# Performance work log

Measured on AMD Instinct MI355X. Metric: run time of the kernel, lower is better.

## Reference

```python
import jax, jax.numpy as jnp
import numpy as np

MARGIN = 0.3
NUM_CLASSES = 1000


def setup_inputs() -> dict:
    key = jax.random.key(0)
    k1, k2 = jax.random.split(key)
    B, D = 8192, 256
    inputs = jax.random.normal(k1, (B, D), dtype=jnp.float32)
    targets = jax.random.randint(k2, (B,), 0, NUM_CLASSES, dtype=jnp.int64)
    return {"inputs": inputs, "targets": targets}


def reference(inputs, targets):
    # Squared Euclidean pairwise distances: ||x_i||^2 + ||x_j||^2 - 2 x_i.x_j
    sq = jnp.sum(inputs * inputs, axis=1)                      # [B]
    dist = sq[:, None] + sq[None, :] - 2.0 * (inputs @ inputs.T)  # [B, B]

    # Hard mining: per-row max over positives (same label, incl. self),
    # min over negatives, exactly as the torch per-row masked max/min loop.
    pos_mask = targets[:, None] == targets[None, :]            # [B, B] bool
    neg_inf = jnp.float32(-jnp.inf)
    pos_inf = jnp.float32(jnp.inf)
    dist_ap = jnp.max(jnp.where(pos_mask, dist, neg_inf), axis=1)  # [B]
    dist_an = jnp.min(jnp.where(pos_mask, pos_inf, dist), axis=1)  # [B]

    # MarginRankingLoss(margin)(dist_an, dist_ap, y=1) = mean relu(ap - an + m)
    loss = jnp.mean(jax.nn.relu(dist_ap - dist_an + MARGIN))
    prec = jnp.mean((dist_an > dist_ap).astype(jnp.float32))
    return (loss, prec)
```

## Files before the change

kernel.cpp:

```cpp
#include <hip/hip_runtime.h>
#include <hip/hip_bf16.h>

#define B_N 8192
#define D_K 256
#define MARGIN 0.3f
#define NBLK 2080

typedef float f32x4 __attribute__((ext_vector_type(4)));
typedef short s16x8 __attribute__((ext_vector_type(8)));

__device__ __forceinline__ unsigned fkey(float f) {
    unsigned u = __float_as_uint(f);
    return (u & 0x80000000u) ? ~u : (u | 0x80000000u);
}
__device__ __forceinline__ float kval(unsigned k) {
    return (k & 0x80000000u) ? __uint_as_float(k ^ 0x80000000u)
                             : __uint_as_float(~k);
}

__device__ __forceinline__ void load_lds16(const unsigned short* g,
                                           unsigned short* l) {
    __builtin_amdgcn_global_load_lds(
        (const __attribute__((address_space(1))) unsigned int*)g,
        (__attribute__((address_space(3))) unsigned int*)l, 16, 0, 0);
}

__device__ __forceinline__ float rowred_max(float v) {
    v = fmaxf(v, __int_as_float(__builtin_amdgcn_update_dpp(
            __float_as_int(v), __float_as_int(v), 0x118, 0xF, 0xF, false)));
    v = fmaxf(v, __int_as_float(__builtin_amdgcn_update_dpp(
            __float_as_int(v), __float_as_int(v), 0x114, 0xF, 0xF, false)));
    v = fmaxf(v, __int_as_float(__builtin_amdgcn_update_dpp(
            __float_as_int(v), __float_as_int(v), 0x112, 0xF, 0xF, false)));
    v = fmaxf(v, __int_as_float(__builtin_amdgcn_update_dpp(
            __float_as_int(v), __float_as_int(v), 0x111, 0xF, 0xF, false)));
    return v;
}
__device__ __forceinline__ float rowred_min(float v) {
    v = fminf(v, __int_as_float(__builtin_amdgcn_update_dpp(
            __float_as_int(v), __float_as_int(v), 0x118, 0xF, 0xF, false)));
    v = fminf(v, __int_as_float(__builtin_amdgcn_update_dpp(
            __float_as_int(v), __float_as_int(v), 0x114, 0xF, 0xF, false)));
    v = fminf(v, __int_as_float(__builtin_amdgcn_update_dpp(
            __float_as_int(v), __float_as_int(v), 0x112, 0xF, 0xF, false)));
    v = fminf(v, __int_as_float(__builtin_amdgcn_update_dpp(
            __float_as_int(v), __float_as_int(v), 0x111, 0xF, 0xF, false)));
    return v;
}

__global__ __launch_bounds__(256) void prep_kernel(const float* __restrict__ X,
        float* __restrict__ sq, unsigned* __restrict__ apk,
        unsigned* __restrict__ ank, unsigned short* __restrict__ Xp,
        float* __restrict__ acc2) {
    int row  = (blockIdx.x << 2) + (threadIdx.x >> 6);
    int lane = threadIdx.x & 63;
    const float4 v = reinterpret_cast<const float4*>(X + (size_t)row * D_K)[lane];

    float xs[4] = {v.x, v.y, v.z, v.w};
    ushort4 hv;
    unsigned short* hp = &hv.x;
    float s = 0.f;
    #pragma unroll
    for (int i = 0; i < 4; ++i) {
        __hip_bfloat16 h = __float2bfloat16(xs[i]);
        hp[i] = *reinterpret_cast<unsigned short*>(&h);
        float hf = __bfloat162float(h);
        s = fmaf(hf, hf, s);
    }
    *reinterpret_cast<ushort4*>(Xp + (size_t)row * D_K + lane * 4) = hv;

    #pragma unroll
    for (int o = 32; o > 0; o >>= 1) s += __shfl_down(s, o, 64);
    if (lane == 0) {
        sq[row]  = s;
        apk[row] = 0u;
        ank[row] = 0xFFFFFFFFu;
    }
    if (blockIdx.x == 0 && threadIdx.x == 0) {
        acc2[0] = 0.f; acc2[1] = 0.f;
        reinterpret_cast<unsigned*>(acc2)[2] = 0u;
    }
}

#define BM 128
#define BN 128

__global__ __launch_bounds__(256, 4) void dist_kernel(
        const unsigned short* __restrict__ Xp,
        const int* __restrict__ tgt, const float* __restrict__ sq,
        unsigned* __restrict__ apk, unsigned* __restrict__ ank) {
    __shared__ unsigned short Ab[2][128 * 32];
    __shared__ unsigned short Bb[2][128 * 32];

    const int t    = threadIdx.x;
    const int lane = t & 63;
    const int wave = t >> 6;
    const int wrow = (wave >> 1) * 64;
    const int wcol = (wave & 1) * 64;
    const int fr   = lane & 15;
    const int quad = lane >> 4;
    const float INF = __int_as_float(0x7f800000);

    int tt = blockIdx.x;
    int bx = (int)((sqrtf(8.f * (float)tt + 1.f) - 1.f) * 0.5f);
    while ((bx + 1) * (bx + 2) / 2 <= tt) ++bx;
    while (bx * (bx + 1) / 2 > tt) --bx;
    int by = tt - bx * (bx + 1) / 2;
    const int bm = by * BM;
    const int bn = bx * BN;

    const unsigned short* ag[2];
    const unsigned short* bg[2];
    int ldso[2];
    #pragma unroll
    for (int j = 0; j < 2; ++j) {
        int S   = wave * 64 + j * 256 + lane;
        int l   = S >> 3, idx = S & 7;
        int u   = idx >> 1, r = l * 2 + (idx & 1);
        ag[j]   = Xp + (size_t)(bm + r) * D_K + u * 8;
        bg[j]   = Xp + (size_t)(bn + r) * D_K + u * 8;
        ldso[j] = S * 8;
    }

    f32x4 acc[4][4];
    #pragma unroll
    for (int i = 0; i < 4; ++i)
        #pragma unroll
        for (int j = 0; j < 4; ++j) acc[i][j] = (f32x4){0.f, 0.f, 0.f, 0.f};

    #pragma unroll
    for (int j = 0; j < 2; ++j) {
        load_lds16(ag[j], &Ab[0][ldso[j]]);
        load_lds16(bg[j], &Bb[0][ldso[j]]);
    }

    #pragma unroll 1
    for (int w = 0; w < 8; ++w) {
        __syncthreads();
        if (w < 7) {
            const int ko = (w + 1) * 32;
            #pragma unroll
            for (int j = 0; j < 2; ++j) {
                load_lds16(ag[j] + ko, &Ab[(w + 1) & 1][ldso[j]]);
                load_lds16(bg[j] + ko, &Bb[(w + 1) & 1][ldso[j]]);
            }
        }
        const unsigned short* At = Ab[w & 1];
        const unsigned short* Bt = Bb[w & 1];

        s16x8 a[4], b[4];
        #pragma unroll
        for (int mi = 0; mi < 4; ++mi) {
            int R = wrow + mi * 16 + fr;
            int S = (R >> 1) * 8 + quad * 2 + (R & 1);
            a[mi] = *reinterpret_cast<const s16x8*>(&At[S * 8]);
        }
        #pragma unroll
        for (int ni = 0; ni < 4; ++ni) {
            int R = wcol + ni * 16 + fr;
            int S = (R >> 1) * 8 + quad * 2 + (R & 1);
            b[ni] = *reinterpret_cast<const s16x8*>(&Bt[S * 8]);
        }
        #pragma unroll
        for (int mi = 0; mi < 4; ++mi)
            #pragma unroll
            for (int ni = 0; ni < 4; ++ni)
                acc[mi][ni] = __builtin_amdgcn_mfma_f32_16x16x32_bf16(
                    a[mi], b[ni], acc[mi][ni], 0, 0, 0);
    }

    int   ct[4]; float csq[4];
    #pragma unroll
    for (int ni = 0; ni < 4; ++ni) {
        int c = bn + wcol + ni * 16 + fr;
        ct[ni] = tgt[c]; csq[ni] = sq[c];
    }
    float cap[4], can[4];
    #pragma unroll
    for (int ni = 0; ni < 4; ++ni) { cap[ni] = -INF; can[ni] = INF; }

    #pragma unroll
    for (int mi = 0; mi < 4; ++mi) {
        #pragma unroll
        for (int reg = 0; reg < 4; ++reg) {
            int rl = wrow + mi * 16 + quad * 4 + reg;
            int rt = tgt[bm + rl]; float rsq = sq[bm + rl];
            float rap = -INF, ran = INF;
            #pragma unroll
            for (int ni = 0; ni < 4; ++ni) {
                float d = rsq + csq[ni] - 2.f * acc[mi][ni][reg];
                bool pos = (rt == ct[ni]);
                if (pos) { rap = fmaxf(rap, d); cap[ni] = fmaxf(cap[ni], d); }
                else     { ran = fminf(ran, d); can[ni] = fminf(can[ni], d); }
            }
            rap = rowred_max(rap);
            ran = rowred_min(ran);
            if (fr == 15) {
                atomicMax(&apk[bm + rl], fkey(rap));
                atomicMin(&ank[bm + rl], fkey(ran));
            }
        }
    }
    #pragma unroll
    for (int ni = 0; ni < 4; ++ni) {
        #pragma unroll
        for (int o = 16; o < 64; o <<= 1) {
            cap[ni] = fmaxf(cap[ni], __shfl_xor(cap[ni], o, 64));
            can[ni] = fminf(can[ni], __shfl_xor(can[ni], o, 64));
        }
    }
    if (lane < 16) {
        #pragma unroll
        for (int ni = 0; ni < 4; ++ni) {
            int c = bn + wcol + ni * 16 + lane;
            atomicMax(&apk[c], fkey(cap[ni]));
            atomicMin(&ank[c], fkey(can[ni]));
        }
    }
}

__global__ __launch_bounds__(256) void final_kernel(const unsigned* __restrict__ apk,
        const unsigned* __restrict__ ank, float* __restrict__ acc2,
        float* __restrict__ out) {
    __shared__ float s_sum[4], s_cnt[4];
    int i = blockIdx.x * 256 + threadIdx.x;
    float ap = kval(apk[i]);
    float an = kval(ank[i]);
    float v  = ap - an + MARGIN;
    float sum = v > 0.f ? v : 0.f;
    float cnt = an > ap ? 1.f : 0.f;
    #pragma unroll
    for (int o = 32; o > 0; o >>= 1) {
        sum += __shfl_down(sum, o, 64);
        cnt += __shfl_down(cnt, o, 64);
    }
    int wave = threadIdx.x >> 6, lane = threadIdx.x & 63;
    if (lane == 0) { s_sum[wave] = sum; s_cnt[wave] = cnt; }
    __syncthreads();
    if (threadIdx.x == 0) {
        float ts = 0.f, tc = 0.f;
        #pragma unroll
        for (int w = 0; w < 4; ++w) { ts += s_sum[w]; tc += s_cnt[w]; }
        atomicAdd(&acc2[0], ts);
        atomicAdd(&acc2[1], tc);
        __threadfence();
        unsigned ticket = atomicAdd(reinterpret_cast<unsigned*>(acc2) + 2, 1u);
        if (ticket == gridDim.x - 1) {
            float fs = atomicAdd(&acc2[0], 0.f);
            float fc = atomicAdd(&acc2[1], 0.f);
            out[0] = fs / (float)B_N;
            out[1] = fc / (float)B_N;
        }
    }
}

extern "C" void kernel_launch(void* const* d_in, const int* in_sizes, int n_in,
                              void* d_out, int out_size, void* d_ws, size_t ws_size,
                              hipStream_t stream) {
    const float* X   = (const float*)d_in[0];
    const int*   tgt = (const int*)d_in[1];

    char* ws = (char*)d_ws;
    float*          sq   = (float*)ws;
    unsigned*       apk  = (unsigned*)(ws + 32768);
    unsigned*       ank  = (unsigned*)(ws + 65536);
    float*          acc2 = (float*)(ws + 98304);
    unsigned short* Xp   = (unsigned short*)(ws + 131072);

    float* out = (float*)d_out;

    prep_kernel<<<B_N / 4, 256, 0, stream>>>(X, sq, apk, ank, Xp, acc2);
    dist_kernel<<<NBLK, 256, 0, stream>>>(Xp, tgt, sq, apk, ank);
    final_kernel<<<B_N / 256, 256, 0, stream>>>(apk, ank, acc2, out);
}
```

Before: 120.2 us.

## Process two triangular tiles per block with continuous prefetch across tiles

Each dist_kernel block now handles two consecutive upper-triangular 128x128 tiles instead of one, halving the grid to 1040 blocks. The k-loop runs 16 steps, so the first K-chunk of the second tile is prefetched into LDS during the last step of the first tile, and the epilogue for the first tile runs while that load is in flight. This is meant to amortize block launch and prologue cost and hide load latency at tile boundaries. In exchange there are fewer blocks to spread over the CUs, which may hurt load balance, and the epilogue inside the loop may raise register pressure.

```diff
diff --git a/kernel.cpp b/kernel.cpp
--- a/kernel.cpp
+++ b/kernel.cpp
@@ -4,7 +4,7 @@
 #define B_N 8192
 #define D_K 256
 #define MARGIN 0.3f
-#define NBLK 2080
+#define NBLK2 1040
 
 typedef float f32x4 __attribute__((ext_vector_type(4)));
 typedef short s16x8 __attribute__((ext_vector_type(8)));
@@ -101,53 +101,64 @@
     const int quad = lane >> 4;
     const float INF = __int_as_float(0x7f800000);
 
-    int tt = blockIdx.x;
+    int tt = blockIdx.x * 2;
     int bx = (int)((sqrtf(8.f * (float)tt + 1.f) - 1.f) * 0.5f);
     while ((bx + 1) * (bx + 2) / 2 <= tt) ++bx;
     while (bx * (bx + 1) / 2 > tt) --bx;
     int by = tt - bx * (bx + 1) / 2;
-    const int bm = by * BM;
-    const int bn = bx * BN;
-
-    const unsigned short* ag[2];
-    const unsigned short* bg[2];
+    int bmA[2], bnA[2];
+    bmA[0] = by * BM; bnA[0] = bx * BN;
+    if (by < bx) { bmA[1] = (by + 1) * BM; bnA[1] = bx * BN; }
+    else         { bmA[1] = 0;             bnA[1] = (bx + 1) * BN; }
+
+    int rgo[2];
+    int ugo[2];
     int ldso[2];
     #pragma unroll
     for (int j = 0; j < 2; ++j) {
         int S   = wave * 64 + j * 256 + lane;
         int l   = S >> 3, idx = S & 7;
-        int u   = idx >> 1, r = l * 2 + (idx & 1);
-        ag[j]   = Xp + (size_t)(bm + r) * D_K + u * 8;
-        bg[j]   = Xp + (size_t)(bn + r) * D_K + u * 8;
+        rgo[j]  = l * 2 + (idx & 1);
+        ugo[j]  = (idx >> 1) * 8;
         ldso[j] = S * 8;
     }
 
     f32x4 acc[4][4];
-    #pragma unroll
-    for (int i = 0; i < 4; ++i)
-        #pragma unroll
-        for (int j = 0; j < 4; ++j) acc[i][j] = (f32x4){0.f, 0.f, 0.f, 0.f};
 
     #pragma unroll
     for (int j = 0; j < 2; ++j) {
-        load_lds16(ag[j], &Ab[0][ldso[j]]);
-        load_lds16(bg[j], &Bb[0][ldso[j]]);
+        load_lds16(Xp + (size_t)(bmA[0] + rgo[j]) * D_K + ugo[j],
+                   &Ab[0][ldso[j]]);
+        load_lds16(Xp + (size_t)(bnA[0] + rgo[j]) * D_K + ugo[j],
+                   &Bb[0][ldso[j]]);
     }
 
     #pragma unroll 1
-    for (int w = 0; w < 8; ++w) {
+    for (int widx = 0; widx < 16; ++widx) {
+        const int w = widx & 7;
         __syncthreads();
-        if (w < 7) {
-            const int ko = (w + 1) * 32;
+        if (widx < 15) {
+            const int nx = widx + 1;
+            const int nt = nx >> 3;
+            const int ko = (nx & 7) * 32;
             #pragma unroll
             for (int j = 0; j < 2; ++j) {
-                load_lds16(ag[j] + ko, &Ab[(w + 1) & 1][ldso[j]]);
-                load_lds16(bg[j] + ko, &Bb[(w + 1) & 1][ldso[j]]);
-            }
-        }
-        const unsigned short* At = Ab[w & 1];
-        const unsigned short* Bt = Bb[w & 1];
-
+                load_lds16(Xp + (size_t)(bmA[nt] + rgo[j]) * D_K + ko + ugo[j],
+                           &Ab[nx & 1][ldso[j]]);
+                load_lds16(Xp + (size_t)(bnA[nt] + rgo[j]) * D_K + ko + ugo[j],
+                           &Bb[nx & 1][ldso[j]]);
+            }
+        }
+        if (w == 0) {
+            #pragma unroll
+            for (int i = 0; i < 4; ++i)
+                #pragma unroll
+                for (int j = 0; j < 4; ++j)
+                    acc[i][j] = (f32x4){0.f, 0.f, 0.f, 0.f};
+        }
+
+        const unsigned short* At = Ab[widx & 1];
+        const unsigned short* Bt = Bb[widx & 1];
         s16x8 a[4], b[4];
         #pragma unroll
         for (int mi = 0; mi < 4; ++mi) {
@@ -167,54 +178,58 @@
             for (int ni = 0; ni < 4; ++ni)
                 acc[mi][ni] = __builtin_amdgcn_mfma_f32_16x16x32_bf16(
                     a[mi], b[ni], acc[mi][ni], 0, 0, 0);
-    }
-
-    int   ct[4]; float csq[4];
-    #pragma unroll
-    for (int ni = 0; ni < 4; ++ni) {
-        int c = bn + wcol + ni * 16 + fr;
-        ct[ni] = tgt[c]; csq[ni] = sq[c];
-    }
-    float cap[4], can[4];
-    #pragma unroll
-    for (int ni = 0; ni < 4; ++ni) { cap[ni] = -INF; can[ni] = INF; }
-
-    #pragma unroll
-    for (int mi = 0; mi < 4; ++mi) {
-        #pragma unroll
-        for (int reg = 0; reg < 4; ++reg) {
-            int rl = wrow + mi * 16 + quad * 4 + reg;
-            int rt = tgt[bm + rl]; float rsq = sq[bm + rl];
-            float rap = -INF, ran = INF;
+
+        if (w == 7) {
+            const int bm = bmA[widx >> 3];
+            const int bn = bnA[widx >> 3];
+            int   ct[4]; float csq[4];
             #pragma unroll
             for (int ni = 0; ni < 4; ++ni) {
-                float d = rsq + csq[ni] - 2.f * acc[mi][ni][reg];
-                bool pos = (rt == ct[ni]);
-                if (pos) { rap = fmaxf(rap, d); cap[ni] = fmaxf(cap[ni], d); }
-                else     { ran = fminf(ran, d); can[ni] = fminf(can[ni], d); }
-            }
-            rap = rowred_max(rap);
-            ran = rowred_min(ran);
-            if (fr == 15) {
-                atomicMax(&apk[bm + rl], fkey(rap));
-                atomicMin(&ank[bm + rl], fkey(ran));
-            }
-        }
-    }
-    #pragma unroll
-    for (int ni = 0; ni < 4; ++ni) {
-        #pragma unroll
-        for (int o = 16; o < 64; o <<= 1) {
-            cap[ni] = fmaxf(cap[ni], __shfl_xor(cap[ni], o, 64));
-            can[ni] = fminf(can[ni], __shfl_xor(can[ni], o, 64));
-        }
-    }
-    if (lane < 16) {
-        #pragma unroll
-        for (int ni = 0; ni < 4; ++ni) {
-            int c = bn + wcol + ni * 16 + lane;
-            atomicMax(&apk[c], fkey(cap[ni]));
-            atomicMin(&ank[c], fkey(can[ni]));
+                int c = bn + wcol + ni * 16 + fr;
+                ct[ni] = tgt[c]; csq[ni] = sq[c];
+            }
+            float cap[4], can[4];
+            #pragma unroll
+            for (int ni = 0; ni < 4; ++ni) { cap[ni] = -INF; can[ni] = INF; }
+
+            #pragma unroll
+            for (int mi = 0; mi < 4; ++mi) {
+                #pragma unroll
+                for (int reg = 0; reg < 4; ++reg) {
+                    int rl = wrow + mi * 16 + quad * 4 + reg;
+                    int rt = tgt[bm + rl]; float rsq = sq[bm + rl];
+                    float rap = -INF, ran = INF;
+                    #pragma unroll
+                    for (int ni = 0; ni < 4; ++ni) {
+                        float d = rsq + csq[ni] - 2.f * acc[mi][ni][reg];
+                        bool pos = (rt == ct[ni]);
+                        if (pos) { rap = fmaxf(rap, d); cap[ni] = fmaxf(cap[ni], d); }
+                        else     { ran = fminf(ran, d); can[ni] = fminf(can[ni], d); }
+                    }
+                    rap = rowred_max(rap);
+                    ran = rowred_min(ran);
+                    if (fr == 15) {
+                        atomicMax(&apk[bm + rl], fkey(rap));
+                        atomicMin(&ank[bm + rl], fkey(ran));
+                    }
+                }
+            }
+            #pragma unroll
+            for (int ni = 0; ni < 4; ++ni) {
+                #pragma unroll
+                for (int o = 16; o < 64; o <<= 1) {
+                    cap[ni] = fmaxf(cap[ni], __shfl_xor(cap[ni], o, 64));
+                    can[ni] = fminf(can[ni], __shfl_xor(can[ni], o, 64));
+                }
+            }
+            if (lane < 16) {
+                #pragma unroll
+                for (int ni = 0; ni < 4; ++ni) {
+                    int c = bn + wcol + ni * 16 + lane;
+                    atomicMax(&apk[c], fkey(cap[ni]));
+                    atomicMin(&ank[c], fkey(can[ni]));
+                }
+            }
         }
     }
 }
@@ -270,6 +285,6 @@
     float* out = (float*)d_out;
 
     prep_kernel<<<B_N / 4, 256, 0, stream>>>(X, sq, apk, ank, Xp, acc2);
-    dist_kernel<<<NBLK, 256, 0, stream>>>(Xp, tgt, sq, apk, ank);
+    dist_kernel<<<NBLK2, 256, 0, stream>>>(Xp, tgt, sq, apk, ank);
     final_kernel<<<B_N / 256, 256, 0, stream>>>(apk, ank, acc2, out);
 }
```

After: 131.4 us. 9.3% more time.

## Use single-wave 64x64 triangular tiles with XOR-swizzled LDS and no block barriers

Applied to the files above, without the earlier changes.

The distance kernel moves from 256-thread blocks on 128x128 tiles to 64-thread single-wave blocks on 64x64 tiles, so the triangular grid grows from 2080 to 8256 tiles. Because each block is one wave, __syncthreads is replaced by explicit s_waitcnt on vmcnt/lgkmcnt, and the last K-step is peeled out of the loop. LDS gets an XOR swizzle to cut bank conflicts. Smaller tiles mean less operand reuse per tile, more global/L2 traffic and roughly twice as many epilogue atomics, traded for finer-grained parallelism and no barrier cost.

```diff
diff --git a/kernel.cpp b/kernel.cpp
--- a/kernel.cpp
+++ b/kernel.cpp
@@ -4,7 +4,7 @@
 #define B_N 8192
 #define D_K 256
 #define MARGIN 0.3f
-#define NBLK 2080
+#define NT 8256
 
 typedef float f32x4 __attribute__((ext_vector_type(4)));
 typedef short s16x8 __attribute__((ext_vector_type(8)));
@@ -82,21 +82,14 @@
     }
 }
 
-#define BM 128
-#define BN 128
-
-__global__ __launch_bounds__(256, 4) void dist_kernel(
+__global__ __launch_bounds__(64, 2) void dist_kernel(
         const unsigned short* __restrict__ Xp,
         const int* __restrict__ tgt, const float* __restrict__ sq,
         unsigned* __restrict__ apk, unsigned* __restrict__ ank) {
-    __shared__ unsigned short Ab[2][128 * 32];
-    __shared__ unsigned short Bb[2][128 * 32];
-
-    const int t    = threadIdx.x;
-    const int lane = t & 63;
-    const int wave = t >> 6;
-    const int wrow = (wave >> 1) * 64;
-    const int wcol = (wave & 1) * 64;
+    __shared__ __attribute__((aligned(16))) unsigned short Ab[2][64 * 32];
+    __shared__ __attribute__((aligned(16))) unsigned short Bb[2][64 * 32];
+
+    const int lane = threadIdx.x;
     const int fr   = lane & 15;
     const int quad = lane >> 4;
     const float INF = __int_as_float(0x7f800000);
@@ -106,22 +99,34 @@
     while ((bx + 1) * (bx + 2) / 2 <= tt) ++bx;
     while (bx * (bx + 1) / 2 > tt) --bx;
     int by = tt - bx * (bx + 1) / 2;
-    const int bm = by * BM;
-    const int bn = bx * BN;
-
-    const unsigned short* ag[2];
-    const unsigned short* bg[2];
-    int ldso[2];
-    #pragma unroll
-    for (int j = 0; j < 2; ++j) {
-        int S   = wave * 64 + j * 256 + lane;
-        int l   = S >> 3, idx = S & 7;
-        int u   = idx >> 1, r = l * 2 + (idx & 1);
-        ag[j]   = Xp + (size_t)(bm + r) * D_K + u * 8;
-        bg[j]   = Xp + (size_t)(bn + r) * D_K + u * 8;
+    const int bm = by * 64;
+    const int bn = bx * 64;
+
+    const unsigned short* ag[4];
+    const unsigned short* bg[4];
+    int ldso[4];
+    #pragma unroll
+    for (int j = 0; j < 4; ++j) {
+        int S = j * 64 + lane;
+        int r = S >> 2;
+        int q = (S & 3) ^ ((r >> 2) & 3);
+        ag[j]   = Xp + (size_t)(bm + r) * D_K + q * 8;
+        bg[j]   = Xp + (size_t)(bn + r) * D_K + q * 8;
         ldso[j] = S * 8;
     }
 
+    int afo[4], bfo[4];
+    #pragma unroll
+    for (int mi = 0; mi < 4; ++mi) {
+        int R = mi * 16 + fr;
+        afo[mi] = (R * 4 + (quad ^ ((R >> 2) & 3))) * 8;
+    }
+    #pragma unroll
+    for (int ni = 0; ni < 4; ++ni) {
+        int R = ni * 16 + fr;
+        bfo[ni] = (R * 4 + (quad ^ ((R >> 2) & 3))) * 8;
+    }
+
     f32x4 acc[4][4];
     #pragma unroll
     for (int i = 0; i < 4; ++i)
@@ -129,38 +134,31 @@
         for (int j = 0; j < 4; ++j) acc[i][j] = (f32x4){0.f, 0.f, 0.f, 0.f};
 
     #pragma unroll
-    for (int j = 0; j < 2; ++j) {
+    for (int j = 0; j < 4; ++j) {
         load_lds16(ag[j], &Ab[0][ldso[j]]);
         load_lds16(bg[j], &Bb[0][ldso[j]]);
     }
 
     #pragma unroll 1
-    for (int w = 0; w < 8; ++w) {
-        __syncthreads();
-        if (w < 7) {
-            const int ko = (w + 1) * 32;
-            #pragma unroll
-            for (int j = 0; j < 2; ++j) {
-                load_lds16(ag[j] + ko, &Ab[(w + 1) & 1][ldso[j]]);
-                load_lds16(bg[j] + ko, &Bb[(w + 1) & 1][ldso[j]]);
-            }
-        }
+    for (int w = 0; w < 7; ++w) {
+        asm volatile("s_waitcnt lgkmcnt(0)" ::: "memory");
+        const int ko = (w + 1) * 32;
+        #pragma unroll
+        for (int j = 0; j < 4; ++j) {
+            load_lds16(ag[j] + ko, &Ab[(w + 1) & 1][ldso[j]]);
+            load_lds16(bg[j] + ko, &Bb[(w + 1) & 1][ldso[j]]);
+        }
+        asm volatile("s_waitcnt vmcnt(8)" ::: "memory");
+
         const unsigned short* At = Ab[w & 1];
         const unsigned short* Bt = Bb[w & 1];
-
         s16x8 a[4], b[4];
         #pragma unroll
-        for (int mi = 0; mi < 4; ++mi) {
-            int R = wrow + mi * 16 + fr;
-            int S = (R >> 1) * 8 + quad * 2 + (R & 1);
-            a[mi] = *reinterpret_cast<const s16x8*>(&At[S * 8]);
-        }
-        #pragma unroll
-        for (int ni = 0; ni < 4; ++ni) {
-            int R = wcol + ni * 16 + fr;
-            int S = (R >> 1) * 8 + quad * 2 + (R & 1);
-            b[ni] = *reinterpret_cast<const s16x8*>(&Bt[S * 8]);
-        }
+        for (int mi = 0; mi < 4; ++mi)
+            a[mi] = *reinterpret_cast<const s16x8*>(&At[afo[mi]]);
+        #pragma unroll
+        for (int ni = 0; ni < 4; ++ni)
+            b[ni] = *reinterpret_cast<const s16x8*>(&Bt[bfo[ni]]);
         #pragma unroll
         for (int mi = 0; mi < 4; ++mi)
             #pragma unroll
@@ -168,11 +166,29 @@
                 acc[mi][ni] = __builtin_amdgcn_mfma_f32_16x16x32_bf16(
                     a[mi], b[ni], acc[mi][ni], 0, 0, 0);
     }
+    {
+        asm volatile("s_waitcnt vmcnt(0)" ::: "memory");
+        const unsigned short* At = Ab[1];
+        const unsigned short* Bt = Bb[1];
+        s16x8 a[4], b[4];
+        #pragma unroll
+        for (int mi = 0; mi < 4; ++mi)
+            a[mi] = *reinterpret_cast<const s16x8*>(&At[afo[mi]]);
+        #pragma unroll
+        for (int ni = 0; ni < 4; ++ni)
+            b[ni] = *reinterpret_cast<const s16x8*>(&Bt[bfo[ni]]);
+        #pragma unroll
+        for (int mi = 0; mi < 4; ++mi)
+            #pragma unroll
+            for (int ni = 0; ni < 4; ++ni)
+                acc[mi][ni] = __builtin_amdgcn_mfma_f32_16x16x32_bf16(
+                    a[mi], b[ni], acc[mi][ni], 0, 0, 0);
+    }
 
     int   ct[4]; float csq[4];
     #pragma unroll
     for (int ni = 0; ni < 4; ++ni) {
-        int c = bn + wcol + ni * 16 + fr;
+        int c = bn + ni * 16 + fr;
         ct[ni] = tgt[c]; csq[ni] = sq[c];
     }
     float cap[4], can[4];
@@ -183,7 +199,7 @@
     for (int mi = 0; mi < 4; ++mi) {
         #pragma unroll
         for (int reg = 0; reg < 4; ++reg) {
-            int rl = wrow + mi * 16 + quad * 4 + reg;
+            int rl = mi * 16 + quad * 4 + reg;
             int rt = tgt[bm + rl]; float rsq = sq[bm + rl];
             float rap = -INF, ran = INF;
             #pragma unroll
@@ -212,7 +228,7 @@
     if (lane < 16) {
         #pragma unroll
         for (int ni = 0; ni < 4; ++ni) {
-            int c = bn + wcol + ni * 16 + lane;
+            int c = bn + ni * 16 + lane;
             atomicMax(&apk[c], fkey(cap[ni]));
             atomicMin(&ank[c], fkey(can[ni]));
         }
@@ -270,6 +286,6 @@
     float* out = (float*)d_out;
 
     prep_kernel<<<B_N / 4, 256, 0, stream>>>(X, sq, apk, ank, Xp, acc2);
-    dist_kernel<<<NBLK, 256, 0, stream>>>(Xp, tgt, sq, apk, ank);
+    dist_kernel<<<NT, 64, 0, stream>>>(Xp, tgt, sq, apk, ank);
     final_kernel<<<B_N / 256, 256, 0, stream>>>(apk, ank, acc2, out);
 }
```

After: 138.4 us. 15.1% more time.
